# Kernel tuning notes

Measured on AMD Instinct MI355X. Metric: run time of the kernel, lower is better.

Reference implementation:

```python
import jax, jax.numpy as jnp
from jax import lax
import numpy as np

B = 32768
N_IN = 8
N_HID = 64
N_CTRL = 2
M_SCEN = (1.0, 1.2)          # scenario parameters for f/g
M_NOM = 1.0
CLF_LAM = 1.0
CBF_LAM = 1.0
P_CLF = 100.0
P_CBF = 50.0
QP_ITERS = 80                # fixed-iteration batched ADMM (OSQP-style) replacing CvxpyLayer
RHO = 1.0
SIGMA = 1e-6
INF = jnp.inf


def setup_inputs() -> dict:
    key = jax.random.key(0)
    ks = jax.random.split(key, 16)
    s = 0.3
    return {
        "x":   jax.random.normal(ks[0], (B, N_IN), jnp.float32),
        "VW1": jax.random.normal(ks[1], (N_HID, N_IN), jnp.float32) * s,
        "Vb1": jax.random.normal(ks[2], (N_HID,), jnp.float32) * s,
        "VW2": jax.random.normal(ks[3], (N_HID, N_HID), jnp.float32) * s,
        "Vb2": jax.random.normal(ks[4], (N_HID,), jnp.float32) * s,
        "HW1": jax.random.normal(ks[5], (N_HID, N_IN), jnp.float32) * s,
        "Hb1": jax.random.normal(ks[6], (N_HID,), jnp.float32) * s,
        "HW2": jax.random.normal(ks[7], (N_HID, N_HID), jnp.float32) * s,
        "Hb2": jax.random.normal(ks[8], (N_HID,), jnp.float32) * s,
        "HW3": jax.random.normal(ks[9], (N_HID, N_HID), jnp.float32) * s,
        "Hb3": jax.random.normal(ks[10], (N_HID,), jnp.float32) * s,
        "HW4": jax.random.normal(ks[11], (1, N_HID), jnp.float32) * s,
        "Hb4": jax.random.normal(ks[12], (1,), jnp.float32) * s,
        "G0":  jax.random.normal(ks[13], (N_IN, N_CTRL), jnp.float32) * s,
        "K":   jax.random.normal(ks[14], (N_IN, N_CTRL), jnp.float32) * s,
    }


def _lyapunov(x, W1, b1, W2, b2):
    t1 = jnp.tanh(x @ W1.T + b1)                                   # [B,H]
    t2 = jnp.tanh(t1 @ W2.T + b2)                                  # [B,H]
    V = 0.5 * jnp.sum(t2 * t2, axis=1)                             # [B]
    # fused diag(1-t^2) @ W chain (no diag_embed materialization)
    D1 = (1.0 - t1 ** 2)[:, :, None] * W1[None]                    # [B,H,N]
    D2 = (1.0 - t2 ** 2)[:, :, None] * jnp.einsum('hk,bkn->bhn', W2, D1)
    grad_V = jnp.einsum('bh,bhn->bn', t2, D2)                      # [B,N]
    return V, grad_V


def _barrier(x, W1, b1, W2, b2, W3, b3, W4, b4):
    t1 = jnp.tanh(x @ W1.T + b1)
    t2 = jnp.tanh(t1 @ W2.T + b2)
    t3 = jnp.tanh(t2 @ W3.T + b3)
    H = t3 @ W4.T + b4                                             # [B,1]
    D1 = (1.0 - t1 ** 2)[:, :, None] * W1[None]
    D2 = (1.0 - t2 ** 2)[:, :, None] * jnp.einsum('hk,bkn->bhn', W2, D1)
    D3 = (1.0 - t3 ** 2)[:, :, None] * jnp.einsum('hk,bkn->bhn', W3, D2)
    grad_H = jnp.einsum('oh,bhn->bn', W4, D3)                      # [B,N] (o=1)
    return H, grad_H


def _solve_qp(q, A, lo, hi):
    """Batched OSQP-style ADMM for min 0.5 z^T P z + q^T z  s.t. lo <= A z <= hi.
    P = diag([2,2,0,0,0,0]); z = [u(2), r_clf(2), s_cbf(2)]. Fixed iterations."""
    nb, mc, nz = A.shape[0], A.shape[1], A.shape[2]
    Pdiag = jnp.array([2.0, 2.0, 0.0, 0.0, 0.0, 0.0], q.dtype)
    M = RHO * jnp.einsum('bmi,bmj->bij', A, A) + jnp.diag(Pdiag + SIGMA)
    Minv = jnp.linalg.inv(M)                                       # [B,6,6]
    x0 = jnp.zeros((nb, nz), q.dtype)
    z0 = jnp.zeros((nb, mc), q.dtype)
    y0 = jnp.zeros((nb, mc), q.dtype)

    def step(carry, _):
        xx, zz, yy = carry
        rhs = SIGMA * xx - q + jnp.einsum('bmi,bm->bi', A, RHO * zz - yy)
        xt = jnp.einsum('bij,bj->bi', Minv, rhs)
        zt = jnp.einsum('bmi,bi->bm', A, xt)
        zn = jnp.clip(zt + yy / RHO, lo, hi)
        yn = yy + RHO * (zt - zn)
        return (xt, zn, yn), None

    (xf, _, _), _ = lax.scan(step, (x0, z0, y0), None, length=QP_ITERS)
    return xf                                                      # [B,6]


def _forward(x, VW1, Vb1, VW2, Vb2, HW1, Hb1, HW2, Hb2, HW3, Hb3, HW4, Hb4, G0, K):
    V, grad_V = _lyapunov(x, VW1, Vb1, VW2, Vb2)
    H, grad_H = _barrier(x, HW1, Hb1, HW2, Hb2, HW3, Hb3, HW4, Hb4)

    LfVs, LgVs, LfHs, LgHs = [], [], [], []
    for m in M_SCEN:
        # f(x,m) = -x/m ; g(x,m) = G0/m
        LfVs.append(-jnp.sum(grad_V * x, axis=1) / m)              # [B]
        LgVs.append((grad_V @ G0) / m)                             # [B,C]
        LfHs.append(-jnp.sum(grad_H * x, axis=1) / m)
        LgHs.append((grad_H @ G0) / m)
    u_nom = -(x @ K) * (1.0 / M_NOM)                               # [B,C]

    nb = x.shape[0]
    z2 = jnp.zeros((nb, 2), x.dtype)
    ey = jnp.eye(2, dtype=x.dtype)
    e = lambda i: jnp.broadcast_to(ey[i], (nb, 2))
    ninf = jnp.full((nb,), -INF, x.dtype)
    pinf = jnp.full((nb,), INF, x.dtype)
    zer = jnp.zeros((nb,), x.dtype)

    rows, los, his = [], [], []
    for i in range(len(M_SCEN)):
        # CBF: LfH + LgH@u + cbf_lam*H + s_i >= 0
        rows.append(jnp.concatenate([LgHs[i], z2, e(i)], axis=1))
        los.append(-(LfHs[i] + CBF_LAM * H[:, 0])); his.append(pinf)
        # CLF: LfV + LgV@u + clf_lam*V - r_i <= 0
        rows.append(jnp.concatenate([LgVs[i], -e(i), z2], axis=1))
        los.append(ninf); his.append(-(LfVs[i] + CLF_LAM * V))
    for i in range(len(M_SCEN)):
        rows.append(jnp.concatenate([z2, e(i), z2], axis=1)); los.append(zer); his.append(pinf)
    for i in range(len(M_SCEN)):
        rows.append(jnp.concatenate([z2, z2, e(i)], axis=1)); los.append(zer); his.append(pinf)

    A = jnp.stack(rows, axis=1)                                    # [B,8,6]
    lo = jnp.stack(los, axis=1)                                    # [B,8]
    hi = jnp.stack(his, axis=1)
    # objective ||u-u_nom||^2 + p_clf*sum r + p_cbf*sum s  ->  q = [-2 u_nom, p_clf, p_clf, p_cbf, p_cbf]
    q = jnp.concatenate([-2.0 * u_nom,
                         jnp.full((nb, 2), P_CLF, x.dtype),
                         jnp.full((nb, 2), P_CBF, x.dtype)], axis=1)

    z = _solve_qp(q, A, lo, hi)                                    # [B,6]
    u = z[:, :N_CTRL]
    relaxation = jnp.mean(z[:, N_CTRL:N_CTRL + len(M_SCEN)], axis=1, keepdims=True)  # [B,1]

    ns = float(len(M_SCEN))
    Vdot = sum(LfVs[i] + jnp.sum(LgVs[i] * u, axis=1) for i in range(len(M_SCEN))) / ns
    Hdot = sum(LfHs[i] + jnp.sum(LgHs[i] * u, axis=1) for i in range(len(M_SCEN))) / ns
    return u, relaxation, V, Vdot[:, None, None], H, Hdot[:, None, None]


def reference(x, VW1, Vb1, VW2, Vb2, HW1, Hb1, HW2, Hb2, HW3, Hb3, HW4, Hb4, G0, K):
    return _forward(x, VW1, Vb1, VW2, Vb2, HW1, Hb1, HW2, Hb2, HW3, Hb3, HW4, Hb4, G0, K)
```

## Files before the change

### kernel.cpp

```cpp
#include <hip/hip_runtime.h>
#include <hip/hip_bf16.h>
#include <math.h>

#define BTOT 32768

typedef _Float16 f16x8 __attribute__((ext_vector_type(8)));
typedef _Float16 f16x4 __attribute__((ext_vector_type(4)));
typedef float    f32x4 __attribute__((ext_vector_type(4)));

#define LDS_FENCE() asm volatile("s_waitcnt lgkmcnt(0)" ::: "memory")

__device__ __forceinline__ float ldin(const void* p, int i, int f32f) {
  return f32f ? ((const float*)p)[i]
              : __bfloat162float(((const __hip_bfloat16*)p)[i]);
}

__device__ __forceinline__ f32x4 MFMA(f16x8 a, f16x8 b, f32x4 c) {
  return __builtin_amdgcn_mfma_f32_16x16x32_f16(a, b, c, 0, 0, 0);
}

__device__ __forceinline__ float tanh_fast(float x) {
  float e = __expf(2.f * x);
  return 1.f - 2.f / (e + 1.f);
}

__device__ __forceinline__ float redq(float v) {
  v += __shfl_xor(v, 16, 64);
  v += __shfl_xor(v, 32, 64);
  return v;
}

__device__ __forceinline__ int widx(int h, int k) {
  return ((h >> 4) << 10) + ((k >> 5) << 9) + (((k >> 3) & 3) << 7) + ((h & 15) << 3) + (k & 7);
}

__global__ __launch_bounds__(512, 2) void fused_kernel(
    const void* px, const void* pVW1, const void* pVb1, const void* pVW2, const void* pVb2,
    const void* pHW1, const void* pHb1, const void* pHW2, const void* pHb2,
    const void* pHW3, const void* pHb3, const void* pHW4, const void* pHb4,
    const void* pG0, const void* pK, float* out)
{
  __shared__ __align__(16) _Float16 sVW2[4096], sVW2T[4096];
  __shared__ __align__(16) _Float16 sHW2[4096], sHW2T[4096];
  __shared__ __align__(16) _Float16 sHW3[4096], sHW3T[4096];
  __shared__ __align__(16) _Float16 sW1Vh[512], sW1Vl[512], sW1Hh[512], sW1Hl[512];
  __shared__ __align__(16) _Float16 sXh[1024], sXl[1024];
  __shared__ __align__(16) _Float16 sAVh[8][1024], sAVl[8][1024];
  __shared__ __align__(16) _Float16 sAHh[8][1024], sAHl[8][1024];
  __shared__ __align__(16) float sVb1[64], sVb2[64], sHb1[64], sHb2[64], sHb3[64], sW4[64];
  __shared__ __align__(16) float sWGV0[64], sWGV1[64], sWGH0[64], sWGH1[64];
  __shared__ __align__(16) float sQP[128][10];
  __shared__ float sKv[16], sHb4v;
  __shared__ int sCnt;

  const int tid = threadIdx.x, lane = tid & 63, wave = tid >> 6;
  const int m = lane & 15, q = lane >> 4;
  const int ro = q * 128 + m * 8;

  if (tid == 0) sCnt = 0;
  __syncthreads();
  {
    const unsigned short* xb = (const unsigned short*)px;
    int good = 0;
#pragma unroll
    for (int i = 0; i < 2; ++i) {
      int ex = (xb[tid * 2 + i] >> 7) & 0xFF;
      good += (ex >= 97 && ex <= 157) ? 1 : 0;
    }
    atomicAdd(&sCnt, good);
  }
  __syncthreads();
  const int f32f = (sCnt >= 870) ? 0 : 1;
  const bool wsplit = (f32f != 0);

  for (int i = tid; i < 4096; i += 512) {
    int h = i >> 6, k = i & 63;
    int fw = widx(h, k), tw = widx(k, h);
    sVW2[fw] = (_Float16)ldin(pVW2, i, f32f); sVW2T[tw] = sVW2[fw];
    sHW2[fw] = (_Float16)ldin(pHW2, i, f32f); sHW2T[tw] = sHW2[fw];
    sHW3[fw] = (_Float16)ldin(pHW3, i, f32f); sHW3T[tw] = sHW3[fw];
  }
  for (int i = tid; i < 512; i += 512) {
    float v = ldin(pVW1, i, f32f); _Float16 hh = (_Float16)v;
    sW1Vh[i] = hh; sW1Vl[i] = (_Float16)(v - (float)hh);
    v = ldin(pHW1, i, f32f); hh = (_Float16)v;
    sW1Hh[i] = hh; sW1Hl[i] = (_Float16)(v - (float)hh);
  }
  for (int i = tid; i < 1024; i += 512) {
    float v = ldin(px, blockIdx.x * 1024 + i, f32f); _Float16 hh = (_Float16)v;
    sXh[i] = hh; sXl[i] = (_Float16)(v - (float)hh);
  }
  if (tid < 64) {
    float a0 = 0.f, a1 = 0.f, b0 = 0.f, b1 = 0.f;
#pragma unroll
    for (int nn = 0; nn < 8; ++nn) {
      float g0 = ldin(pG0, 2 * nn, f32f), g1 = ldin(pG0, 2 * nn + 1, f32f);
      float wv = ldin(pVW1, tid * 8 + nn, f32f), wh = ldin(pHW1, tid * 8 + nn, f32f);
      a0 += wv * g0; a1 += wv * g1; b0 += wh * g0; b1 += wh * g1;
    }
    sWGV0[tid] = a0; sWGV1[tid] = a1; sWGH0[tid] = b0; sWGH1[tid] = b1;
    sVb1[tid] = ldin(pVb1, tid, f32f);
    sVb2[tid] = ldin(pVb2, tid, f32f);
    sHb1[tid] = ldin(pHb1, tid, f32f);
    sHb2[tid] = ldin(pHb2, tid, f32f);
    sHb3[tid] = ldin(pHb3, tid, f32f);
    sW4[tid]  = ldin(pHW4, tid, f32f);
  }
  if (tid < 16) sKv[tid] = ldin(pK, tid, f32f);
  if (tid == 0) sHb4v = ldin(pHb4, 0, f32f);
  __syncthreads();

  f16x8 zf;
#pragma unroll
  for (int i = 0; i < 8; ++i) zf[i] = (_Float16)0.f;

  _Float16 *aVh = sAVh[wave], *aVl = sAVl[wave];
  _Float16 *aHh = sAHh[wave], *aHl = sAHl[wave];
  const int tb = wave * 16;

  auto wgemm = [&](const _Float16* Wp, const _Float16* ah_, const _Float16* al_, f32x4* acc) {
    f16x8 b0h = *(const f16x8*)(ah_ + ro);
    f16x8 b1h = *(const f16x8*)(ah_ + 512 + ro);
    f16x8 b0l = *(const f16x8*)(al_ + ro);
    f16x8 b1l = *(const f16x8*)(al_ + 512 + ro);
#pragma unroll
    for (int ht = 0; ht < 4; ++ht) {
      const _Float16* ap = Wp + ht * 1024 + ro;
      f16x8 a0 = *(const f16x8*)ap, a1 = *(const f16x8*)(ap + 512);
      f32x4 c = {0.f, 0.f, 0.f, 0.f};
      c = MFMA(a0, b0h, c); c = MFMA(a1, b1h, c);
      c = MFMA(a0, b0l, c); c = MFMA(a1, b1l, c);
      acc[ht] = c;
    }
  };
  auto wstore = [&](const f32x4* vals, _Float16* ah_, _Float16* al_) {
#pragma unroll
    for (int ht = 0; ht < 4; ++ht) {
      int aw = ((ht >> 1) << 9) + (((ht & 1) * 2 + (q >> 1)) << 7) + m * 8 + ((q & 1) << 2);
      f16x4 vh, vl;
#pragma unroll
      for (int r = 0; r < 4; ++r) {
        float x = vals[ht][r];
        _Float16 hh = (_Float16)x;
        vh[r] = hh; vl[r] = (_Float16)(x - (float)hh);
      }
      *(f16x4*)(ah_ + aw) = vh;
      *(f16x4*)(al_ + aw) = vl;
    }
  };
  auto l1gemm = [&](const _Float16* W1h, const _Float16* W1l, f32x4* acc) {
    f16x8 xbh = zf, xbl = zf;
    if (lane < 16) {
      xbh = *(const f16x8*)(sXh + (tb + m) * 8);
      xbl = *(const f16x8*)(sXl + (tb + m) * 8);
    }
#pragma unroll
    for (int ht = 0; ht < 4; ++ht) {
      f16x8 afh = zf, afl = zf;
      if (lane < 16) {
        afh = *(const f16x8*)(W1h + (ht * 16 + m) * 8);
        afl = *(const f16x8*)(W1l + (ht * 16 + m) * 8);
      }
      f32x4 c = {0.f, 0.f, 0.f, 0.f};
      c = MFMA(afh, xbh, c);
      c = MFMA(afh, xbl, c);
      if (wsplit) c = MFMA(afl, xbh, c);
      acc[ht] = c;
    }
  };

  f32x4 accV[4], accH[4], z1V[4], z1H[4], d1V[4], d1H[4], d2H[4], tvV[4], tvH[4];

  l1gemm(sW1Vh, sW1Vl, accV);
  l1gemm(sW1Hh, sW1Hl, accH);
#pragma unroll
  for (int ht = 0; ht < 4; ++ht) {
    z1V[ht] = accV[ht]; z1H[ht] = accH[ht];
    f32x4 bV = *(const f32x4*)&sVb1[ht * 16 + q * 4];
    f32x4 bH = *(const f32x4*)&sHb1[ht * 16 + q * 4];
#pragma unroll
    for (int r = 0; r < 4; ++r) {
      float t = tanh_fast(z1V[ht][r] + bV[r]);
      tvV[ht][r] = t; d1V[ht][r] = 1.f - t * t;
      t = tanh_fast(z1H[ht][r] + bH[r]);
      tvH[ht][r] = t; d1H[ht][r] = 1.f - t * t;
    }
  }
  wstore(tvV, aVh, aVl);
  wstore(tvH, aHh, aHl);
  LDS_FENCE();

  wgemm(sVW2, aVh, aVl, accV);
  wgemm(sHW2, aHh, aHl, accH);
  float pV = 0.f;
#pragma unroll
  for (int ht = 0; ht < 4; ++ht) {
    f32x4 bV = *(const f32x4*)&sVb2[ht * 16 + q * 4];
    f32x4 bH = *(const f32x4*)&sHb2[ht * 16 + q * 4];
#pragma unroll
    for (int r = 0; r < 4; ++r) {
      float t = tanh_fast(accV[ht][r] + bV[r]);
      pV += t * t;
      tvV[ht][r] = t * (1.f - t * t);
      t = tanh_fast(accH[ht][r] + bH[r]);
      tvH[ht][r] = t; d2H[ht][r] = 1.f - t * t;
    }
  }
  wstore(tvV, aVh, aVl);
  wstore(tvH, aHh, aHl);
  LDS_FENCE();

  wgemm(sVW2T, aVh, aVl, accV);
  wgemm(sHW3, aHh, aHl, accH);
  float pgvx = 0.f, plv0 = 0.f, plv1 = 0.f, pH = 0.f;
#pragma unroll
  for (int ht = 0; ht < 4; ++ht) {
    f32x4 g0 = *(const f32x4*)&sWGV0[ht * 16 + q * 4];
    f32x4 g1 = *(const f32x4*)&sWGV1[ht * 16 + q * 4];
    f32x4 bH = *(const f32x4*)&sHb3[ht * 16 + q * 4];
    f32x4 w4 = *(const f32x4*)&sW4[ht * 16 + q * 4];
#pragma unroll
    for (int r = 0; r < 4; ++r) {
      float wt = accV[ht][r] * d1V[ht][r];
      pgvx += wt * z1V[ht][r];
      plv0 += wt * g0[r]; plv1 += wt * g1[r];
      float t = tanh_fast(accH[ht][r] + bH[r]);
      pH += t * w4[r];
      tvH[ht][r] = w4[r] * (1.f - t * t);
    }
  }
  wstore(tvH, aHh, aHl);
  LDS_FENCE();

  wgemm(sHW3T, aHh, aHl, accH);
#pragma unroll
  for (int ht = 0; ht < 4; ++ht)
#pragma unroll
    for (int r = 0; r < 4; ++r) tvH[ht][r] = accH[ht][r] * d2H[ht][r];
  wstore(tvH, aHh, aHl);
  LDS_FENCE();

  wgemm(sHW2T, aHh, aHl, accH);
  float pghx = 0.f, plh0 = 0.f, plh1 = 0.f;
#pragma unroll
  for (int ht = 0; ht < 4; ++ht) {
    f32x4 g0 = *(const f32x4*)&sWGH0[ht * 16 + q * 4];
    f32x4 g1 = *(const f32x4*)&sWGH1[ht * 16 + q * 4];
#pragma unroll
    for (int r = 0; r < 4; ++r) {
      float wt = accH[ht][r] * d1H[ht][r];
      pghx += wt * z1H[ht][r];
      plh0 += wt * g0[r]; plh1 += wt * g1[r];
    }
  }

  {
    float rgvx = redq(pgvx), rlv0 = redq(plv0), rlv1 = redq(plv1), rV = 0.5f * redq(pV);
    float rghx = redq(pghx), rlh0 = redq(plh0), rlh1 = redq(plh1), rH = redq(pH) + sHb4v;
    if (lane < 16) {
      int el = tb + lane;
      sQP[el][0] = rlh0;  sQP[el][1] = rlh1;
      sQP[el][2] = rlv0;  sQP[el][3] = rlv1;
      sQP[el][4] = rghx;  sQP[el][5] = rgvx;
      sQP[el][6] = rV;    sQP[el][7] = rH;
    }
  }
  __syncthreads();

  if (tid >= 128) return;
  const int e = blockIdx.x * 128 + tid;
  const float im = 1.0f / 1.2f;
  const float sg = 1e-6f;

  float gh0 = sQP[tid][0], gh1 = sQP[tid][1];
  float gv0 = sQP[tid][2], gv1 = sQP[tid][3];
  float ghx = sQP[tid][4], gvx = sQP[tid][5];
  float V   = sQP[tid][6], H   = sQP[tid][7];
  float un0 = 0.f, un1 = 0.f;
#pragma unroll
  for (int n = 0; n < 8; ++n) {
    float xv = (float)sXh[tid * 8 + n] + (float)sXl[tid * 8 + n];
    un0 -= xv * sKv[2 * n];
    un1 -= xv * sKv[2 * n + 1];
  }

  float lo0 = ghx - H;
  float hi1 = gvx - V;
  float lo2 = ghx * im - H;
  float hi3 = gvx * im - V;

  float qv[6] = { -2.f * un0, -2.f * un1, 100.f, 100.f, 50.f, 50.f };

  float Mm[6][6];
#pragma unroll
  for (int r = 0; r < 6; ++r)
#pragma unroll
    for (int c = 0; c < 6; ++c) Mm[r][c] = 0.f;
  const float al = 1.f + im * im;
  Mm[0][0] = al * (gh0 * gh0 + gv0 * gv0) + 2.f + sg;
  Mm[1][1] = al * (gh1 * gh1 + gv1 * gv1) + 2.f + sg;
  Mm[0][1] = Mm[1][0] = al * (gh0 * gh1 + gv0 * gv1);
  Mm[0][2] = Mm[2][0] = -gv0;       Mm[1][2] = Mm[2][1] = -gv1;
  Mm[0][3] = Mm[3][0] = -gv0 * im;  Mm[1][3] = Mm[3][1] = -gv1 * im;
  Mm[0][4] = Mm[4][0] = gh0;        Mm[1][4] = Mm[4][1] = gh1;
  Mm[0][5] = Mm[5][0] = gh0 * im;   Mm[1][5] = Mm[5][1] = gh1 * im;
  Mm[2][2] = Mm[3][3] = Mm[4][4] = Mm[5][5] = 2.f + sg;

  float Iv[6][6];
#pragma unroll
  for (int r = 0; r < 6; ++r)
#pragma unroll
    for (int c = 0; c < 6; ++c) Iv[r][c] = (r == c) ? 1.f : 0.f;
#pragma unroll
  for (int p = 0; p < 6; ++p) {
    float pv = 1.f / Mm[p][p];
#pragma unroll
    for (int c = 0; c < 6; ++c) { Mm[p][c] *= pv; Iv[p][c] *= pv; }
#pragma unroll
    for (int r = 0; r < 6; ++r) {
      if (r == p) continue;
      float f = Mm[r][p];
#pragma unroll
      for (int c = 0; c < 6; ++c) { Mm[r][c] -= f * Mm[p][c]; Iv[r][c] -= f * Iv[p][c]; }
    }
  }

  float X[6] = {0.f, 0.f, 0.f, 0.f, 0.f, 0.f};
  float Z[8] = {0.f, 0.f, 0.f, 0.f, 0.f, 0.f, 0.f, 0.f};
  float Y[8] = {0.f, 0.f, 0.f, 0.f, 0.f, 0.f, 0.f, 0.f};

#pragma unroll 1
  for (int it = 0; it < 80; ++it) {
    float t0 = Z[0] - Y[0], t1 = Z[1] - Y[1], t2 = Z[2] - Y[2], t3 = Z[3] - Y[3];
    float t4 = Z[4] - Y[4], t5 = Z[5] - Y[5], t6 = Z[6] - Y[6], t7 = Z[7] - Y[7];
    float r0 = gh0 * t0 + gv0 * t1 + gh0 * im * t2 + gv0 * im * t3;
    float r1 = gh1 * t0 + gv1 * t1 + gh1 * im * t2 + gv1 * im * t3;
    float r2 = -t1 + t4;
    float r3 = -t3 + t5;
    float r4 =  t0 + t6;
    float r5 =  t2 + t7;
    float rhs[6] = { sg * X[0] - qv[0] + r0, sg * X[1] - qv[1] + r1,
                     sg * X[2] - qv[2] + r2, sg * X[3] - qv[3] + r3,
                     sg * X[4] - qv[4] + r4, sg * X[5] - qv[5] + r5 };
#pragma unroll
    for (int i = 0; i < 6; ++i) {
      float s = 0.f;
#pragma unroll
      for (int jj = 0; jj < 6; ++jj) s += Iv[i][jj] * rhs[jj];
      X[i] = s;
    }
    float gdH = gh0 * X[0] + gh1 * X[1];
    float gdV = gv0 * X[0] + gv1 * X[1];
    float zt0 = gdH + X[4];
    float zt1 = gdV - X[2];
    float zt2 = gdH * im + X[5];
    float zt3 = gdV * im - X[3];
    float zt4 = X[2], zt5 = X[3], zt6 = X[4], zt7 = X[5];

    float v, zn;
    v = zt0 + Y[0]; zn = fmaxf(v, lo0); Y[0] += zt0 - zn; Z[0] = zn;
    v = zt1 + Y[1]; zn = fminf(v, hi1); Y[1] += zt1 - zn; Z[1] = zn;
    v = zt2 + Y[2]; zn = fmaxf(v, lo2); Y[2] += zt2 - zn; Z[2] = zn;
    v = zt3 + Y[3]; zn = fminf(v, hi3); Y[3] += zt3 - zn; Z[3] = zn;
    v = zt4 + Y[4]; zn = fmaxf(v, 0.f); Y[4] += zt4 - zn; Z[4] = zn;
    v = zt5 + Y[5]; zn = fmaxf(v, 0.f); Y[5] += zt5 - zn; Z[5] = zn;
    v = zt6 + Y[6]; zn = fmaxf(v, 0.f); Y[6] += zt6 - zn; Z[6] = zn;
    v = zt7 + Y[7]; zn = fmaxf(v, 0.f); Y[7] += zt7 - zn; Z[7] = zn;
  }

  float u0 = X[0], u1 = X[1];
  float relax = 0.5f * (X[2] + X[3]);
  const float cc = 0.5f * (1.f + im);
  float Vdot = cc * (gv0 * u0 + gv1 * u1 - gvx);
  float Hdot = cc * (gh0 * u0 + gh1 * u1 - ghx);

  out[2 * e]      = u0;
  out[2 * e + 1]  = u1;
  out[65536 + e]  = relax;
  out[98304 + e]  = V;
  out[131072 + e] = Vdot;
  out[163840 + e] = H;
  out[196608 + e] = Hdot;
}

extern "C" void kernel_launch(void* const* d_in, const int* in_sizes, int n_in,
                              void* d_out, int out_size, void* d_ws, size_t ws_size,
                              hipStream_t stream) {
  float* out = (float*)d_out;
  fused_kernel<<<256, 512, 0, stream>>>(
      d_in[0], d_in[1], d_in[2], d_in[3], d_in[4],
      d_in[5], d_in[6], d_in[7], d_in[8],
      d_in[9], d_in[10], d_in[11], d_in[12],
      d_in[13], d_in[14], out);
}
```

Baseline: 118.6 us.

## Split QP solve into separate kernel and use Schur-complement closed-form solve

Splits the fused kernel in two. The network kernel writes per-element gradients to a workspace, and a second kernel runs the 80-iteration ADMM loop with 64-thread blocks across 512 blocks, so the QP phase no longer idles 3/4 of each 512-thread block. The explicit 6x6 inverse is replaced by a Schur-complement solve that exploits the diagonal structure, which cuts per-iteration arithmetic and register pressure. In exchange it adds a second launch and a global-memory round trip for the intermediate values.

Result: slower. 122.3 us (+3.1%).

```diff
diff --git a/kernel.cpp b/kernel.cpp
--- a/kernel.cpp
+++ b/kernel.cpp
@@ -34,11 +34,11 @@
   return ((h >> 4) << 10) + ((k >> 5) << 9) + (((k >> 3) & 3) << 7) + ((h & 15) << 3) + (k & 7);
 }
 
-__global__ __launch_bounds__(512, 2) void fused_kernel(
+__global__ __launch_bounds__(512, 2) void nn_kernel(
     const void* px, const void* pVW1, const void* pVb1, const void* pVW2, const void* pVb2,
     const void* pHW1, const void* pHb1, const void* pHW2, const void* pHb2,
     const void* pHW3, const void* pHb3, const void* pHW4, const void* pHb4,
-    const void* pG0, const void* pK, float* out)
+    const void* pG0, const void* pK, float* WS, float* out)
 {
   __shared__ __align__(16) _Float16 sVW2[4096], sVW2T[4096];
   __shared__ __align__(16) _Float16 sHW2[4096], sHW2T[4096];
@@ -49,8 +49,7 @@
   __shared__ __align__(16) _Float16 sAHh[8][1024], sAHl[8][1024];
   __shared__ __align__(16) float sVb1[64], sVb2[64], sHb1[64], sHb2[64], sHb3[64], sW4[64];
   __shared__ __align__(16) float sWGV0[64], sWGV1[64], sWGH0[64], sWGH1[64];
-  __shared__ __align__(16) float sQP[128][10];
-  __shared__ float sKv[16], sHb4v;
+  __shared__ float sHb4v;
   __shared__ int sCnt;
 
   const int tid = threadIdx.x, lane = tid & 63, wave = tid >> 6;
@@ -106,7 +105,6 @@
     sHb3[tid] = ldin(pHb3, tid, f32f);
     sW4[tid]  = ldin(pHW4, tid, f32f);
   }
-  if (tid < 16) sKv[tid] = ldin(pK, tid, f32f);
   if (tid == 0) sHb4v = ldin(pHb4, 0, f32f);
   __syncthreads();
 
@@ -258,74 +256,69 @@
     float rgvx = redq(pgvx), rlv0 = redq(plv0), rlv1 = redq(plv1), rV = 0.5f * redq(pV);
     float rghx = redq(pghx), rlh0 = redq(plh0), rlh1 = redq(plh1), rH = redq(pH) + sHb4v;
     if (lane < 16) {
-      int el = tb + lane;
-      sQP[el][0] = rlh0;  sQP[el][1] = rlh1;
-      sQP[el][2] = rlv0;  sQP[el][3] = rlv1;
-      sQP[el][4] = rghx;  sQP[el][5] = rgvx;
-      sQP[el][6] = rV;    sQP[el][7] = rH;
-    }
-  }
-  __syncthreads();
-
-  if (tid >= 128) return;
-  const int e = blockIdx.x * 128 + tid;
+      int e = blockIdx.x * 128 + tb + lane;
+      WS[0 * BTOT + e] = rlh0;  WS[1 * BTOT + e] = rlh1;
+      WS[2 * BTOT + e] = rlv0;  WS[3 * BTOT + e] = rlv1;
+      WS[4 * BTOT + e] = rghx;  WS[5 * BTOT + e] = rgvx;
+      out[98304 + e]  = rV;
+      out[163840 + e] = rH;
+    }
+  }
+}
+
+__global__ __launch_bounds__(64) void qp_kernel(const void* px, const void* pK,
+                                                const float* WS, float* out) {
+  __shared__ int sCnt;
+  const int tid = threadIdx.x;
+  if (tid == 0) sCnt = 0;
+  __syncthreads();
+  {
+    const unsigned short* xb = (const unsigned short*)px;
+    int good = 0;
+#pragma unroll
+    for (int i = 0; i < 2; ++i) {
+      int ex = (xb[tid * 2 + i] >> 7) & 0xFF;
+      good += (ex >= 97 && ex <= 157) ? 1 : 0;
+    }
+    atomicAdd(&sCnt, good);
+  }
+  __syncthreads();
+  const int f32f = (sCnt >= 109) ? 0 : 1;
+
+  const int e = blockIdx.x * 64 + tid;
   const float im = 1.0f / 1.2f;
   const float sg = 1e-6f;
 
-  float gh0 = sQP[tid][0], gh1 = sQP[tid][1];
-  float gv0 = sQP[tid][2], gv1 = sQP[tid][3];
-  float ghx = sQP[tid][4], gvx = sQP[tid][5];
-  float V   = sQP[tid][6], H   = sQP[tid][7];
+  float gh0 = WS[0 * BTOT + e], gh1 = WS[1 * BTOT + e];
+  float gv0 = WS[2 * BTOT + e], gv1 = WS[3 * BTOT + e];
+  float ghx = WS[4 * BTOT + e], gvx = WS[5 * BTOT + e];
+  float V = out[98304 + e], H = out[163840 + e];
+
   float un0 = 0.f, un1 = 0.f;
 #pragma unroll
   for (int n = 0; n < 8; ++n) {
-    float xv = (float)sXh[tid * 8 + n] + (float)sXl[tid * 8 + n];
-    un0 -= xv * sKv[2 * n];
-    un1 -= xv * sKv[2 * n + 1];
+    float xv = ldin(px, e * 8 + n, f32f);
+    un0 -= xv * ldin(pK, 2 * n, f32f);
+    un1 -= xv * ldin(pK, 2 * n + 1, f32f);
   }
 
   float lo0 = ghx - H;
   float hi1 = gvx - V;
   float lo2 = ghx * im - H;
   float hi3 = gvx * im - V;
-
-  float qv[6] = { -2.f * un0, -2.f * un1, 100.f, 100.f, 50.f, 50.f };
-
-  float Mm[6][6];
-#pragma unroll
-  for (int r = 0; r < 6; ++r)
-#pragma unroll
-    for (int c = 0; c < 6; ++c) Mm[r][c] = 0.f;
+  float qv0 = -2.f * un0, qv1 = -2.f * un1;
+
+  const float d  = 2.f + sg;
+  const float rd = 1.f / d;
   const float al = 1.f + im * im;
-  Mm[0][0] = al * (gh0 * gh0 + gv0 * gv0) + 2.f + sg;
-  Mm[1][1] = al * (gh1 * gh1 + gv1 * gv1) + 2.f + sg;
-  Mm[0][1] = Mm[1][0] = al * (gh0 * gh1 + gv0 * gv1);
-  Mm[0][2] = Mm[2][0] = -gv0;       Mm[1][2] = Mm[2][1] = -gv1;
-  Mm[0][3] = Mm[3][0] = -gv0 * im;  Mm[1][3] = Mm[3][1] = -gv1 * im;
-  Mm[0][4] = Mm[4][0] = gh0;        Mm[1][4] = Mm[4][1] = gh1;
-  Mm[0][5] = Mm[5][0] = gh0 * im;   Mm[1][5] = Mm[5][1] = gh1 * im;
-  Mm[2][2] = Mm[3][3] = Mm[4][4] = Mm[5][5] = 2.f + sg;
-
-  float Iv[6][6];
-#pragma unroll
-  for (int r = 0; r < 6; ++r)
-#pragma unroll
-    for (int c = 0; c < 6; ++c) Iv[r][c] = (r == c) ? 1.f : 0.f;
-#pragma unroll
-  for (int p = 0; p < 6; ++p) {
-    float pv = 1.f / Mm[p][p];
-#pragma unroll
-    for (int c = 0; c < 6; ++c) { Mm[p][c] *= pv; Iv[p][c] *= pv; }
-#pragma unroll
-    for (int r = 0; r < 6; ++r) {
-      if (r == p) continue;
-      float f = Mm[r][p];
-#pragma unroll
-      for (int c = 0; c < 6; ++c) { Mm[r][c] -= f * Mm[p][c]; Iv[r][c] -= f * Iv[p][c]; }
-    }
-  }
-
-  float X[6] = {0.f, 0.f, 0.f, 0.f, 0.f, 0.f};
+  const float be = al * (1.f - rd);
+  float S00 = be * (gh0 * gh0 + gv0 * gv0) + d;
+  float S11 = be * (gh1 * gh1 + gv1 * gv1) + d;
+  float S01 = be * (gh0 * gh1 + gv0 * gv1);
+  float idet = 1.f / (S00 * S11 - S01 * S01);
+  float i00 = S11 * idet, i11 = S00 * idet, i01 = -S01 * idet;
+
+  float X0 = 0.f, X1 = 0.f, X2 = 0.f, X3 = 0.f, X4 = 0.f, X5 = 0.f;
   float Z[8] = {0.f, 0.f, 0.f, 0.f, 0.f, 0.f, 0.f, 0.f};
   float Y[8] = {0.f, 0.f, 0.f, 0.f, 0.f, 0.f, 0.f, 0.f};
 
@@ -333,53 +326,52 @@
   for (int it = 0; it < 80; ++it) {
     float t0 = Z[0] - Y[0], t1 = Z[1] - Y[1], t2 = Z[2] - Y[2], t3 = Z[3] - Y[3];
     float t4 = Z[4] - Y[4], t5 = Z[5] - Y[5], t6 = Z[6] - Y[6], t7 = Z[7] - Y[7];
-    float r0 = gh0 * t0 + gv0 * t1 + gh0 * im * t2 + gv0 * im * t3;
-    float r1 = gh1 * t0 + gv1 * t1 + gh1 * im * t2 + gv1 * im * t3;
-    float r2 = -t1 + t4;
-    float r3 = -t3 + t5;
-    float r4 =  t0 + t6;
-    float r5 =  t2 + t7;
-    float rhs[6] = { sg * X[0] - qv[0] + r0, sg * X[1] - qv[1] + r1,
-                     sg * X[2] - qv[2] + r2, sg * X[3] - qv[3] + r3,
-                     sg * X[4] - qv[4] + r4, sg * X[5] - qv[5] + r5 };
-#pragma unroll
-    for (int i = 0; i < 6; ++i) {
-      float s = 0.f;
-#pragma unroll
-      for (int jj = 0; jj < 6; ++jj) s += Iv[i][jj] * rhs[jj];
-      X[i] = s;
-    }
-    float gdH = gh0 * X[0] + gh1 * X[1];
-    float gdV = gv0 * X[0] + gv1 * X[1];
-    float zt0 = gdH + X[4];
-    float zt1 = gdV - X[2];
-    float zt2 = gdH * im + X[5];
-    float zt3 = gdV * im - X[3];
-    float zt4 = X[2], zt5 = X[3], zt6 = X[4], zt7 = X[5];
+    float tauh = t0 + im * t2, tauv = t1 + im * t3;
+    float b0 = sg * X0 - qv0 + gh0 * tauh + gv0 * tauv;
+    float b1 = sg * X1 - qv1 + gh1 * tauh + gv1 * tauv;
+    float b2 = sg * X2 - 100.f - t1 + t4;
+    float b3 = sg * X3 - 100.f - t3 + t5;
+    float b4 = sg * X4 - 50.f + t0 + t6;
+    float b5 = sg * X5 - 50.f + t2 + t7;
+    float p  = b2 + im * b3;
+    float s2 = b4 + im * b5;
+    float cb0 = gh0 * s2 - gv0 * p;
+    float cb1 = gh1 * s2 - gv1 * p;
+    float u0b = b0 - cb0 * rd;
+    float u1b = b1 - cb1 * rd;
+    X0 = i00 * u0b + i01 * u1b;
+    X1 = i01 * u0b + i11 * u1b;
+    float gdH = gh0 * X0 + gh1 * X1;
+    float gdV = gv0 * X0 + gv1 * X1;
+    X2 = (b2 + gdV) * rd;
+    X3 = (b3 + im * gdV) * rd;
+    X4 = (b4 - gdH) * rd;
+    X5 = (b5 - im * gdH) * rd;
+    float zt0 = gdH + X4;
+    float zt1 = gdV - X2;
+    float zt2 = gdH * im + X5;
+    float zt3 = gdV * im - X3;
 
     float v, zn;
     v = zt0 + Y[0]; zn = fmaxf(v, lo0); Y[0] += zt0 - zn; Z[0] = zn;
     v = zt1 + Y[1]; zn = fminf(v, hi1); Y[1] += zt1 - zn; Z[1] = zn;
     v = zt2 + Y[2]; zn = fmaxf(v, lo2); Y[2] += zt2 - zn; Z[2] = zn;
     v = zt3 + Y[3]; zn = fminf(v, hi3); Y[3] += zt3 - zn; Z[3] = zn;
-    v = zt4 + Y[4]; zn = fmaxf(v, 0.f); Y[4] += zt4 - zn; Z[4] = zn;
-    v = zt5 + Y[5]; zn = fmaxf(v, 0.f); Y[5] += zt5 - zn; Z[5] = zn;
-    v = zt6 + Y[6]; zn = fmaxf(v, 0.f); Y[6] += zt6 - zn; Z[6] = zn;
-    v = zt7 + Y[7]; zn = fmaxf(v, 0.f); Y[7] += zt7 - zn; Z[7] = zn;
-  }
-
-  float u0 = X[0], u1 = X[1];
-  float relax = 0.5f * (X[2] + X[3]);
+    v = X2 + Y[4];  zn = fmaxf(v, 0.f); Y[4] += X2 - zn;  Z[4] = zn;
+    v = X3 + Y[5];  zn = fmaxf(v, 0.f); Y[5] += X3 - zn;  Z[5] = zn;
+    v = X4 + Y[6];  zn = fmaxf(v, 0.f); Y[6] += X4 - zn;  Z[6] = zn;
+    v = X5 + Y[7];  zn = fmaxf(v, 0.f); Y[7] += X5 - zn;  Z[7] = zn;
+  }
+
+  float relax = 0.5f * (X2 + X3);
   const float cc = 0.5f * (1.f + im);
-  float Vdot = cc * (gv0 * u0 + gv1 * u1 - gvx);
-  float Hdot = cc * (gh0 * u0 + gh1 * u1 - ghx);
-
-  out[2 * e]      = u0;
-  out[2 * e + 1]  = u1;
+  float Vdot = cc * (gv0 * X0 + gv1 * X1 - gvx);
+  float Hdot = cc * (gh0 * X0 + gh1 * X1 - ghx);
+
+  out[2 * e]      = X0;
+  out[2 * e + 1]  = X1;
   out[65536 + e]  = relax;
-  out[98304 + e]  = V;
   out[131072 + e] = Vdot;
-  out[163840 + e] = H;
   out[196608 + e] = Hdot;
 }
 
@@ -387,9 +379,11 @@
                               void* d_out, int out_size, void* d_ws, size_t ws_size,
                               hipStream_t stream) {
   float* out = (float*)d_out;
-  fused_kernel<<<256, 512, 0, stream>>>(
+  float* WS  = (float*)d_ws;
+  nn_kernel<<<256, 512, 0, stream>>>(
       d_in[0], d_in[1], d_in[2], d_in[3], d_in[4],
       d_in[5], d_in[6], d_in[7], d_in[8],
       d_in[9], d_in[10], d_in[11], d_in[12],
-      d_in[13], d_in[14], out);
-}
+      d_in[13], d_in[14], WS, out);
+  qp_kernel<<<512, 64, 0, stream>>>(d_in[0], d_in[14], WS, out);
+}
```
